# Kernel tuning notes

Measured on AMD Instinct MI355X. Metric: run time of the kernel, lower is better.

The kernel has to match this reference:

```python
import jax, jax.numpy as jnp
import numpy as np

B, N, L, D = 4096, 11, 12, 256
ZDIM = 32
LINE_DIM = 64
PAST_DIM = 6 * D - (2 * D + LINE_DIM)  # 960


def _pos_enc(length, d):
    # PositionalAgentEncoding.build_pos_enc
    pos = jnp.arange(length, dtype=jnp.float32)[:, None]
    div = jnp.exp(jnp.arange(0, d, 2, dtype=jnp.float32) * (-np.log(10000.0) / d))
    pe = jnp.zeros((length, d), dtype=jnp.float32)
    pe = pe.at[:, 0::2].set(jnp.sin(pos * div))
    pe = pe.at[:, 1::2].set(jnp.cos(pos * div))
    return pe


def setup_inputs() -> dict:
    key = jax.random.key(0)
    ks = jax.random.split(key, 16)
    s = 0.02
    return {
        "inputs": jax.random.normal(ks[0], (B * N, L, 4), jnp.float32),
        "past_feature": jax.random.normal(ks[1], (B * N, PAST_DIM), jnp.float32),
        "W_in": jax.random.normal(ks[2], (4, D), jnp.float32) * s,
        "b_in": jnp.zeros((D,), jnp.float32),
        "W_pos": jax.random.normal(ks[3], (2 * D, D), jnp.float32) * s,
        "b_pos": jnp.zeros((D,), jnp.float32),
        "W_fc2": jax.random.normal(ks[4], (L * D, D), jnp.float32) * s,
        "b_fc2": jnp.zeros((D,), jnp.float32),
        "W_fc3": jax.random.normal(ks[5], (D + N, D), jnp.float32) * s,
        "b_fc3": jnp.zeros((D,), jnp.float32),
        "W_msg": jax.random.normal(ks[6], (2 * D, D), jnp.float32) * s,
        "b_msg": jnp.zeros((D,), jnp.float32),
        "W_hyp": jax.random.normal(ks[7], (2 * D, D), jnp.float32) * s,
        "b_hyp": jnp.zeros((D,), jnp.float32),
        "W_line": jax.random.normal(ks[8], (D, LINE_DIM), jnp.float32) * s,
        "W_out": jax.random.normal(ks[9], (6 * D, 128), jnp.float32) * s,
        "b_out": jnp.zeros((128,), jnp.float32),
        "W_qz": jax.random.normal(ks[10], (128, 2 * ZDIM), jnp.float32) * s,
        "b_qz": jnp.zeros((2 * ZDIM,), jnp.float32),
        "batch_size": B,
        "agent_num": N,
    }


def reference(inputs, past_feature, W_in, b_in, W_pos, b_pos, W_fc2, b_fc2,
              W_fc3, b_fc3, W_msg, b_msg, W_hyp, b_hyp, W_line,
              W_out, b_out, W_qz, b_qz, batch_size, agent_num):
    BN, length, _ = inputs.shape
    d = W_in.shape[1]
    bsz, n = batch_size, agent_num
    # input_fc + positional encoding (concat=True, dropout=eval identity)
    tf = inputs @ W_in + b_in                                   # [BN, L, D]
    pe = jnp.broadcast_to(_pos_enc(length, d), (BN, length, d))
    tf = jnp.concatenate([tf, pe], axis=-1) @ W_pos + b_pos     # [BN, L, D]
    # input_fc2 over flattened time, then category concat + input_fc3
    ftraj = tf.reshape(bsz, n, length * d) @ W_fc2 + b_fc2      # [B, N, D]
    cat = jnp.broadcast_to(jnp.eye(n, dtype=ftraj.dtype), (bsz, n, n))
    ftraj = jnp.concatenate([ftraj, cat], axis=-1) @ W_fc3 + b_fc3
    # cosine correlation + per-scene adaptive threshold
    q = ftraj / jnp.linalg.norm(ftraj, axis=2, keepdims=True)
    corr = jnp.einsum('bnd,bmd->bnm', q, q)                     # [B, N, N]
    a = corr.min(axis=(1, 2))
    thr = jnp.where(a < 0.4, 0.4,
                    jnp.where((a > 0.4) & (a < 0.6), a + 0.1, a + 0.03))
    corr = jnp.where(corr < thr[:, None, None], 0.0, corr)
    # ordinary MS_HGNN surrogate: one dense message-passing round
    attn = jax.nn.softmax(jnp.einsum('bnd,bmd->bnm', ftraj, ftraj)
                          / jnp.sqrt(jnp.asarray(d, ftraj.dtype)), axis=-1)
    agg = jnp.einsum('bnm,bmd->bnd', attn, ftraj)
    ftraj_inter = jax.nn.relu(jnp.concatenate([ftraj, agg], -1) @ W_msg + b_msg)
    # hyper/clique surrogate: binarized thresholded corr as incidence, degree-normalized
    A = (corr > 0).astype(ftraj.dtype)
    A = A / jnp.maximum(A.sum(-1, keepdims=True), 1.0)
    hag = jnp.einsum('bnm,bmd->bnd', A, ftraj)
    hyp = jax.nn.relu(jnp.concatenate([ftraj, hag], -1) @ W_hyp + b_hyp)
    feat_bs = hyp @ W_line                                      # [B, N, 64]
    final = jnp.concatenate([ftraj, ftraj_inter, feat_bs], -1).reshape(bsz * n, -1)
    h = jnp.concatenate([past_feature, final], axis=-1)         # [BN, 6D]
    h = jax.nn.relu(h @ W_out + b_out)
    return h @ W_qz + b_qz                                      # [BN, 2*zdim]
```

## Files before the change

kernel.cpp:

```cpp
#include <hip/hip_runtime.h>
#include <hip/hip_bf16.h>

#define BB 4096
#define NNA 11
#define BN (BB*NNA)

#define OFF_WEFF   0
#define OFF_BIASL  1024
#define OFF_WBIG   4096
#define OFF_BIAS2  16384
#define OFF_WALL   16640
#define OFF_BIASN  28928
#define OFF_WG1F   31744
#define OFF_BIASG1 87040
#define OFF_WG2    99712
#define OFF_WQT    198656
#define OFF_P2T    202752
#define OFF_P3T    205824
#define OFF_MIX    296320
#define OFF_INTER  1287552

typedef short bh8 __attribute__((ext_vector_type(8)));
typedef float fx4 __attribute__((ext_vector_type(4)));

__device__ __forceinline__ float b2f(__hip_bfloat16 x) { return __bfloat162float(x); }
__device__ __forceinline__ short f2bs(float v) { __hip_bfloat16 h = __float2bfloat16(v); return *(short*)&h; }


__global__ __launch_bounds__(256) void k_p1(const float* W_in, const float* b_in,
                                            const float* W_pos, const float* b_pos,
                                            float* ws) {
  __shared__ float A[16*512];
  __shared__ float red[4*16*64];
  int t = threadIdx.x, cb = blockIdx.x;
  int ks = t >> 6, c = t & 63, col = cb*64 + c;
  float coef = -logf(10000.f) / 256.f;
  for (int i = t; i < 16*512; i += 256) {
    int row = i >> 9, kk = i & 511;
    float v;
    if (row < 4) v = (kk < 256) ? W_in[row*256 + kk] : 0.f;
    else if (kk < 256) v = b_in[kk];
    else {
      int ii = (kk - 256) >> 1;
      float dv = expf(coef * (float)(2*ii));
      float ang = (float)(row - 4) * dv;
      v = (kk & 1) ? cosf(ang) : sinf(ang);
    }
    A[i] = v;
  }
  __syncthreads();
  float acc[16];
  #pragma unroll
  for (int r = 0; r < 16; ++r) acc[r] = 0.f;
  #pragma unroll 4
  for (int j = 0; j < 128; ++j) {
    int jj = ks*128 + j;
    float b = W_pos[(size_t)jj*256 + col];
    #pragma unroll
    for (int r = 0; r < 16; ++r) acc[r] += A[r*512 + jj] * b;
  }
  #pragma unroll
  for (int r = 0; r < 16; ++r) red[(ks*16 + r)*64 + c] = acc[r];
  __syncthreads();
  for (int i = t; i < 16*64; i += 256) {
    int row = i >> 6, cc = i & 63;
    float s = red[row*64+cc] + red[(16+row)*64+cc] + red[(32+row)*64+cc] + red[(48+row)*64+cc];
    int gcol = cb*64 + cc;
    if (row < 4) ws[OFF_WEFF + row*256 + gcol] = s;
    else         ws[OFF_BIASL + (row-4)*256 + gcol] = s + b_pos[gcol];
  }
}

__global__ __launch_bounds__(256) void k_p2(const float* W_fc2, float* ws) {
  __shared__ float A[5*256];
  __shared__ float red[4*5*64];
  int t = threadIdx.x, cb = blockIdx.x, l = blockIdx.y;
  int ks = t >> 6, c = t & 63, col = cb*64 + c;
  for (int i = t; i < 5*256; i += 256) {
    int row = i >> 8, kk = i & 255;
    A[i] = (row < 4) ? ws[OFF_WEFF + row*256 + kk] : ws[OFF_BIASL + l*256 + kk];
  }
  __syncthreads();
  float acc[5] = {0.f, 0.f, 0.f, 0.f, 0.f};
  #pragma unroll 4
  for (int j = 0; j < 64; ++j) {
    int jj = ks*64 + j;
    float b = W_fc2[(size_t)(l*256 + jj)*256 + col];
    #pragma unroll
    for (int r = 0; r < 5; ++r) acc[r] += A[r*256 + jj] * b;
  }
  #pragma unroll
  for (int r = 0; r < 5; ++r) red[(ks*5 + r)*64 + c] = acc[r];
  __syncthreads();
  for (int i = t; i < 5*64; i += 256) {
    int row = i / 64, cc = i % 64;
    float s = red[row*64+cc] + red[(5+row)*64+cc] + red[(10+row)*64+cc] + red[(15+row)*64+cc];
    int gcol = cb*64 + cc;
    if (row < 4) ws[OFF_WBIG + (l*4 + row)*256 + gcol] = s;
    else         ws[OFF_P2T + l*256 + gcol] = s;
  }
}

__global__ __launch_bounds__(256) void k_p2b(const float* b_fc2, float* ws) {
  int d = threadIdx.x;
  float s = b_fc2[d];
  #pragma unroll
  for (int l = 0; l < 12; ++l) s += ws[OFF_P2T + l*256 + d];
  ws[OFF_BIAS2 + d] = s;
}

__global__ __launch_bounds__(256) void k_p3(const float* W_fc3, float* ws) {
  __shared__ float A[7*256];
  __shared__ float red[4*7*64];
  int t = threadIdx.x, cb = blockIdx.x, rg = blockIdx.y;
  int ks = t >> 6, c = t & 63, col = cb*64 + c;
  for (int i = t; i < 7*256; i += 256) {
    int row = i >> 8, kk = i & 255, gr = rg*7 + row;
    A[i] = (gr < 48) ? ws[OFF_WBIG + gr*256 + kk] : (gr == 48 ? ws[OFF_BIAS2 + kk] : 0.f);
  }
  __syncthreads();
  float acc[7] = {0.f,0.f,0.f,0.f,0.f,0.f,0.f};
  #pragma unroll 4
  for (int j = 0; j < 64; ++j) {
    int jj = ks*64 + j;
    float b = W_fc3[(size_t)jj*256 + col];
    #pragma unroll
    for (int r = 0; r < 7; ++r) acc[r] += A[r*256 + jj] * b;
  }
  #pragma unroll
  for (int r = 0; r < 7; ++r) red[(ks*7 + r)*64 + c] = acc[r];
  __syncthreads();
  for (int i = t; i < 7*64; i += 256) {
    int row = i / 64, cc = i % 64, gr = rg*7 + row;
    float s = red[row*64+cc] + red[(7+row)*64+cc] + red[(14+row)*64+cc] + red[(21+row)*64+cc];
    int gcol = cb*64 + cc;
    if (gr < 48)       ws[OFF_WALL + gr*256 + gcol] = s;
    else if (gr == 48) ws[OFF_P3T + gcol] = s;
  }
}

__global__ __launch_bounds__(256) void k_p3b(const float* W_fc3, const float* b_fc3, float* ws) {
  int d = threadIdx.x, n = blockIdx.x;
  ws[OFF_BIASN + n*256 + d] = ws[OFF_P3T + d] + b_fc3[d] + W_fc3[(size_t)(256+n)*256 + d];
}

__device__ __forceinline__ float wg1_elem(int j, int col, const float* W_msg,
                                          const float* W_hyp, const float* W_out) {
  if (col < 256)       return W_msg[j*256 + col];
  else if (col < 512)  return W_msg[(256+j)*256 + (col-256)];
  else if (col < 768)  return W_hyp[j*256 + (col-512)];
  else if (col < 1024) return W_hyp[(256+j)*256 + (col-768)];
  else                 return W_out[(960+j)*128 + (col-1024)];
}

__global__ __launch_bounds__(256) void k_p4(const float* W_msg, const float* b_msg,
                                            const float* W_hyp, const float* b_hyp,
                                            const float* W_out, float* ws) {
  __shared__ float A[8*256];
  __shared__ float red[4*8*64];
  int t = threadIdx.x, cb = blockIdx.x, rg = blockIdx.y;
  int ks = t >> 6, c = t & 63, col = cb*64 + c;
  for (int i = t; i < 8*256; i += 256) {
    int row = i >> 8, kk = i & 255, gr = rg*8 + row;
    A[i] = (gr < 48) ? ws[OFF_WALL + gr*256 + kk]
         : (gr < 59 ? ws[OFF_BIASN + (gr-48)*256 + kk] : 0.f);
  }
  __syncthreads();
  float acc[8];
  #pragma unroll
  for (int r = 0; r < 8; ++r) acc[r] = 0.f;
  #pragma unroll 4
  for (int j = 0; j < 64; ++j) {
    int jj = ks*64 + j;
    float b = wg1_elem(jj, col, W_msg, W_hyp, W_out);
    #pragma unroll
    for (int r = 0; r < 8; ++r) acc[r] += A[r*256 + jj] * b;
  }
  #pragma unroll
  for (int r = 0; r < 8; ++r) red[(ks*8 + r)*64 + c] = acc[r];
  __syncthreads();
  for (int i = t; i < 8*64; i += 256) {
    int row = i >> 6, cc = i & 63, gr = rg*8 + row;
    float s = red[row*64+cc] + red[(8+row)*64+cc] + red[(16+row)*64+cc] + red[(24+row)*64+cc];
    int gcol = cb*64 + cc;
    if (gr < 48) {
      ws[OFF_WG1F + gr*1152 + gcol] = s;
    } else if (gr < 59) {
      if (gcol < 256) s += b_msg[gcol];
      else if (gcol >= 512 && gcol < 768) s += b_hyp[gcol-512];
      ws[OFF_BIASG1 + (gr-48)*1152 + gcol] = s;
    }
  }
}

__global__ __launch_bounds__(128) void k_p5(const float* W_line, const float* W_out,
                                            float* ws) {
  int c = threadIdx.x, r = blockIdx.x;
  float v;
  if (r < 960)       v = W_out[r*128 + c];
  else if (r < 1216) v = W_out[(r+256)*128 + c];
  else if (r < 1472) {
    int dd = r - 1216;
    float s = 0.f;
    for (int j = 0; j < 64; ++j)
      s += W_line[dd*64 + j] * W_out[(1472+j)*128 + c];
    v = s;
  } else if (r < 1520) {
    v = ws[OFF_WG1F + (r-1472)*1152 + 1024 + c];
  } else v = 0.f;
  short* WTs = (short*)(ws + OFF_WG2);
  WTs[(size_t)c*1536 + r] = f2bs(v);
}

__global__ __launch_bounds__(256) void k_p6(const float* W_qz, float* ws) {
  int i = blockIdx.x*256 + threadIdx.x;
  int n = i >> 7, k = i & 127;
  short* WQs = (short*)(ws + OFF_WQT);
  WQs[n*128 + k] = f2bs(W_qz[k*64 + n]);
}

__global__ __launch_bounds__(256) void k_front(const float* inputs, float* ws) {
  __shared__ float XT[48*44];
  __shared__ float F[44*260];
  __shared__ float C[4*121];
  int t = threadIdx.x;
  int R0 = blockIdx.x * 44;
  for (int i = t; i < 44*48; i += 256) {
    int r = i / 48, k = i - r*48;
    XT[k*44 + r] = inputs[(size_t)(R0+r)*48 + k];
  }
  __syncthreads();
  {
    int d = t;
    float acc[44];
    #pragma unroll
    for (int r = 0; r < 44; ++r) acc[r] = ws[OFF_BIASN + (r % 11)*256 + d];
    for (int k = 0; k < 48; ++k) {
      float w = ws[OFF_WALL + k*256 + d];
      #pragma unroll
      for (int j = 0; j < 11; ++j) {
        float4 xv = *(const float4*)&XT[k*44 + 4*j];
        acc[4*j+0] += xv.x*w; acc[4*j+1] += xv.y*w;
        acc[4*j+2] += xv.z*w; acc[4*j+3] += xv.w*w;
      }
    }
    #pragma unroll
    for (int r = 0; r < 44; ++r) F[r*260 + d] = acc[r];
  }
  __syncthreads();
  int w = t >> 6, lane = t & 63;
  {
    const float4* F4 = (const float4*)F;
    for (int p = lane; p < 66; p += 64) {
      int n = 0, pp = p;
      while (pp >= 11 - n) { pp -= 11 - n; ++n; }
      int m = n + pp;
      int ra = (w*11 + n) * 65, rb2 = (w*11 + m) * 65;
      float s = 0.f;
      #pragma unroll 4
      for (int j = 0; j < 64; ++j) {
        float4 a = F4[ra + j], b = F4[rb2 + j];
        s += a.x*b.x + a.y*b.y + a.z*b.z + a.w*b.w;
      }
      C[w*121 + n*11 + m] = s;
      C[w*121 + m*11 + n] = s;
    }
  }
  __syncthreads();
  {
    float* Cw = C + w*121;
    float rn[11];
    #pragma unroll
    for (int n = 0; n < 11; ++n) rn[n] = 1.f / sqrtf(Cw[n*11+n]);
    float a = 1e30f;
    for (int n = 0; n < 11; ++n)
      for (int m = 0; m < 11; ++m)
        a = fminf(a, Cw[n*11+m] * rn[n] * rn[m]);
    float thr = (a < 0.4f) ? 0.4f : (((a > 0.4f) && (a < 0.6f)) ? a + 0.1f : a + 0.03f);
    int scene = blockIdx.x*4 + w;
    float* mixb = ws + OFF_MIX + (size_t)scene*242;
    if (lane < 11) {
      int n = lane;
      float mx = -1e30f;
      #pragma unroll
      for (int m = 0; m < 11; ++m) mx = fmaxf(mx, Cw[n*11+m]);
      mx *= (1.f/16.f);
      float e[11], ssum = 0.f;
      #pragma unroll
      for (int m = 0; m < 11; ++m) { e[m] = expf(Cw[n*11+m]*(1.f/16.f) - mx); ssum += e[m]; }
      float inv = 1.f / ssum;
      #pragma unroll
      for (int m = 0; m < 11; ++m) mixb[n*11+m] = e[m]*inv;
      float keep[11], cnt = 0.f;
      #pragma unroll
      for (int m = 0; m < 11; ++m) {
        float q = Cw[n*11+m] * rn[n] * rn[m];
        keep[m] = (q >= thr) ? 1.f : 0.f; cnt += keep[m];
      }
      float sc = 1.f / fmaxf(cnt, 1.f);
      #pragma unroll
      for (int m = 0; m < 11; ++m) mixb[121 + n*11 + m] = keep[m]*sc;
    }
  }
}

__global__ __launch_bounds__(256) void k_mix(const float* inputs, float* ws,
                                             __hip_bfloat16* outI, __hip_bfloat16* outH) {
  __shared__ float XT[48*24];
  __shared__ float MW[2*121];
  int t = threadIdx.x;
  int s0 = blockIdx.x * 2;
  int R0 = s0 * 11;
  int gy = blockIdx.y;
  __hip_bfloat16* dst = gy ? outH : outI;
  for (int i = t; i < 22*48; i += 256) {
    int r = i / 48, k = i - r*48;
    XT[k*24 + r] = inputs[(size_t)(R0+r)*48 + k];
  }
  for (int i = t; i < 96; i += 256) { int k = i >> 1, r = 22 + (i & 1); XT[k*24+r] = 0.f; }
  for (int i = t; i < 242; i += 256) {
    int s = i / 121, j = i - s*121;
    MW[i] = ws[OFF_MIX + (size_t)(s0+s)*242 + gy*121 + j];
  }
  __syncthreads();
  int gc = gy*512 + t;
  float accT[24], accB[24];
  #pragma unroll
  for (int r = 0; r < 24; ++r) {
    if (r < 22) {
      accT[r] = ws[OFF_BIASG1 + (r % 11)*1152 + gc];
      accB[r] = ws[OFF_BIASG1 + (r % 11)*1152 + gc + 256];
    } else { accT[r] = 0.f; accB[r] = 0.f; }
  }
  for (int k = 0; k < 48; ++k) {
    float wt = ws[OFF_WG1F + k*1152 + gc];
    float wb = ws[OFF_WG1F + k*1152 + gc + 256];
    #pragma unroll
    for (int j = 0; j < 6; ++j) {
      float4 xv = *(const float4*)&XT[k*24 + 4*j];
      accT[4*j+0] += xv.x*wt; accT[4*j+1] += xv.y*wt; accT[4*j+2] += xv.z*wt; accT[4*j+3] += xv.w*wt;
      accB[4*j+0] += xv.x*wb; accB[4*j+1] += xv.y*wb; accB[4*j+2] += xv.z*wb; accB[4*j+3] += xv.w*wb;
    }
  }
  #pragma unroll
  for (int s = 0; s < 2; ++s)
    #pragma unroll
    for (int n = 0; n < 11; ++n) {
      float v = accT[s*11+n];
      #pragma unroll
      for (int m = 0; m < 11; ++m)
        v += MW[s*121 + n*11 + m] * accB[s*11+m];
      v = fmaxf(v, 0.f);
      dst[(size_t)(R0 + s*11 + n)*256 + t] = __float2bfloat16(v);
    }
}

#define A_OFF 0
#define BT_OFF 4608
#define HS_OFF 0
#define WQ_OFF 8704
__global__ __launch_bounds__(256) void k_g2(const float* past, const float* inputs,
                                            const float* b_out, const float* b_qz,
                                            const __hip_bfloat16* interI, const __hip_bfloat16* hypI,
                                            float* ws, float* out) {
  __shared__ short LDS[18432];
  int t = threadIdx.x;
  int R0 = blockIdx.x * 64;
  int w = t >> 6, lane = t & 63, quad = lane >> 4, l16 = lane & 15;
  const short* WTs = (const short*)(ws + OFF_WG2);
  const short* WQs = (const short*)(ws + OFF_WQT);
  const short* intS = (const short*)interI;
  const short* hypS = (const short*)hypI;

  fx4 acc[4][2];
  #pragma unroll
  for (int mt = 0; mt < 4; ++mt)
    #pragma unroll
    for (int reg = 0; reg < 4; ++reg) {
      int nidx = (R0 + mt*16 + quad*4 + reg) % 11;
      #pragma unroll
      for (int nt = 0; nt < 2; ++nt) {
        int col = w*32 + nt*16 + l16;
        acc[mt][nt][reg] = b_out[col] + ws[OFF_BIASG1 + nidx*1152 + 1024 + col];
      }
    }

  int ar = t >> 2, akq = (t & 3) * 16;
  int bn = t >> 1, bkh = (t & 1) * 32;
  for (int ch = 0; ch < 24; ++ch) {
    __syncthreads();
    {
      short tmp[16];
      if (ch < 15) {
        const float4* sp = (const float4*)(past + (size_t)(R0+ar)*960 + ch*64 + akq);
        #pragma unroll
        for (int q = 0; q < 4; ++q) {
          float4 v = sp[q];
          tmp[4*q+0]=f2bs(v.x); tmp[4*q+1]=f2bs(v.y); tmp[4*q+2]=f2bs(v.z); tmp[4*q+3]=f2bs(v.w);
        }
        *(bh8*)&LDS[A_OFF + ar*72 + akq]     = *(bh8*)&tmp[0];
        *(bh8*)&LDS[A_OFF + ar*72 + akq + 8] = *(bh8*)&tmp[8];
      } else if (ch < 23) {
        const short* s = ((ch < 19) ? intS : hypS) + (size_t)(R0+ar)*256 + ((ch < 19) ? (ch-15) : (ch-19))*64 + akq;
        *(bh8*)&LDS[A_OFF + ar*72 + akq]     = *(const bh8*)&s[0];
        *(bh8*)&LDS[A_OFF + ar*72 + akq + 8] = *(const bh8*)&s[8];
      } else {
        if (akq < 48) {
          const float4* sp = (const float4*)(inputs + (size_t)(R0+ar)*48 + akq);
          #pragma unroll
          for (int q = 0; q < 4; ++q) {
            float4 v = sp[q];
            tmp[4*q+0]=f2bs(v.x); tmp[4*q+1]=f2bs(v.y); tmp[4*q+2]=f2bs(v.z); tmp[4*q+3]=f2bs(v.w);
          }
        } else {
          #pragma unroll
          for (int q = 0; q < 16; ++q) tmp[q] = 0;
        }
        *(bh8*)&LDS[A_OFF + ar*72 + akq]     = *(bh8*)&tmp[0];
        *(bh8*)&LDS[A_OFF + ar*72 + akq + 8] = *(bh8*)&tmp[8];
      }
    }
    {
      const short* s = WTs + (size_t)bn*1536 + ch*64 + bkh;
      #pragma unroll
      for (int q = 0; q < 4; ++q)
        *(bh8*)&LDS[BT_OFF + bn*72 + bkh + q*8] = *(const bh8*)&s[q*8];
    }
    __syncthreads();
    #pragma unroll
    for (int ks = 0; ks < 2; ++ks) {
      int kk = ks*32 + quad*8;
      bh8 a[4], b[2];
      #pragma unroll
      for (int mt = 0; mt < 4; ++mt) a[mt] = *(const bh8*)&LDS[A_OFF + (mt*16 + l16)*72 + kk];
      #pragma unroll
      for (int nt = 0; nt < 2; ++nt) b[nt] = *(const bh8*)&LDS[BT_OFF + (w*32 + nt*16 + l16)*72 + kk];
      #pragma unroll
      for (int mt = 0; mt < 4; ++mt)
        #pragma unroll
        for (int nt = 0; nt < 2; ++nt)
          acc[mt][nt] = __builtin_amdgcn_mfma_f32_16x16x32_bf16(a[mt], b[nt], acc[mt][nt], 0, 0, 0);
    }
  }
  __syncthreads();
  #pragma unroll
  for (int mt = 0; mt < 4; ++mt)
    #pragma unroll
    for (int nt = 0; nt < 2; ++nt)
      #pragma unroll
      for (int reg = 0; reg < 4; ++reg)
        LDS[HS_OFF + (mt*16 + quad*4 + reg)*136 + w*32 + nt*16 + l16] = f2bs(fmaxf(acc[mt][nt][reg], 0.f));
  {
    int n = t >> 2, kh = (t & 3) * 32;
    const short* s = WQs + n*128 + kh;
    #pragma unroll
    for (int q = 0; q < 4; ++q)
      *(bh8*)&LDS[WQ_OFF + n*136 + kh + q*8] = *(const bh8*)&s[q*8];
  }
  __syncthreads();
  fx4 acc2[4];
  {
    float bq = b_qz[w*16 + l16];
    #pragma unroll
    for (int mt = 0; mt < 4; ++mt) { acc2[mt][0]=bq; acc2[mt][1]=bq; acc2[mt][2]=bq; acc2[mt][3]=bq; }
  }
  #pragma unroll
  for (int ks = 0; ks < 4; ++ks) {
    int kk = ks*32 + quad*8;
    bh8 bb = *(const bh8*)&LDS[WQ_OFF + (w*16 + l16)*136 + kk];
    #pragma unroll
    for (int mt = 0; mt < 4; ++mt) {
      bh8 aa = *(const bh8*)&LDS[HS_OFF + (mt*16 + l16)*136 + kk];
      acc2[mt] = __builtin_amdgcn_mfma_f32_16x16x32_bf16(aa, bb, acc2[mt], 0, 0, 0);
    }
  }
  #pragma unroll
  for (int mt = 0; mt < 4; ++mt)
    #pragma unroll
    for (int reg = 0; reg < 4; ++reg)
      out[(size_t)(R0 + mt*16 + quad*4 + reg)*64 + w*16 + l16] = acc2[mt][reg];
}

extern "C" void kernel_launch(void* const* d_in, const int* in_sizes, int n_in,
                              void* d_out, int out_size, void* d_ws, size_t ws_size,
                              hipStream_t stream) {
  const float* inputs = (const float*)d_in[0];
  const float* past   = (const float*)d_in[1];
  const float* W_in   = (const float*)d_in[2];
  const float* b_in   = (const float*)d_in[3];
  const float* W_pos  = (const float*)d_in[4];
  const float* b_pos  = (const float*)d_in[5];
  const float* W_fc2  = (const float*)d_in[6];
  const float* b_fc2  = (const float*)d_in[7];
  const float* W_fc3  = (const float*)d_in[8];
  const float* b_fc3  = (const float*)d_in[9];
  const float* W_msg  = (const float*)d_in[10];
  const float* b_msg  = (const float*)d_in[11];
  const float* W_hyp  = (const float*)d_in[12];
  const float* b_hyp  = (const float*)d_in[13];
  const float* W_line = (const float*)d_in[14];
  const float* W_out  = (const float*)d_in[15];
  const float* b_out  = (const float*)d_in[16];
  const float* W_qz   = (const float*)d_in[17];
  const float* b_qz   = (const float*)d_in[18];
  float* ws = (float*)d_ws;
  __hip_bfloat16* interI = (__hip_bfloat16*)(ws + OFF_INTER);
  __hip_bfloat16* hypI   = interI + (size_t)BN*256;
  float* outp   = (float*)d_out;

  hipLaunchKernelGGL(k_p1,  dim3(4),      dim3(256), 0, stream, W_in, b_in, W_pos, b_pos, ws);
  hipLaunchKernelGGL(k_p2,  dim3(4, 12),  dim3(256), 0, stream, W_fc2, ws);
  hipLaunchKernelGGL(k_p2b, dim3(1),      dim3(256), 0, stream, b_fc2, ws);
  hipLaunchKernelGGL(k_p3,  dim3(4, 7),   dim3(256), 0, stream, W_fc3, ws);
  hipLaunchKernelGGL(k_p3b, dim3(11),     dim3(256), 0, stream, W_fc3, b_fc3, ws);
  hipLaunchKernelGGL(k_p4,  dim3(18, 8),  dim3(256), 0, stream, W_msg, b_msg, W_hyp, b_hyp, W_out, ws);
  hipLaunchKernelGGL(k_p5,  dim3(1536),   dim3(128), 0, stream, W_line, W_out, ws);
  hipLaunchKernelGGL(k_p6,  dim3(32),     dim3(256), 0, stream, W_qz, ws);
  hipLaunchKernelGGL(k_front, dim3(1024), dim3(256), 0, stream, inputs, ws);
  hipLaunchKernelGGL(k_mix, dim3(2048, 2), dim3(256), 0, stream, inputs, ws, interI, hypI);
  hipLaunchKernelGGL(k_g2,  dim3(704),    dim3(256), 0, stream, past, inputs, b_out, b_qz,
                     interI, hypI, ws, outp);
}
```

Baseline: 517.0 us.

## Double-buffer k_g2 GEMM with direct global-to-LDS loads and fold prep kernels

The main GEMM in k_g2 now double-buffers its A and B tiles in LDS. It uses XOR-swizzled layouts, stages the B operand with global_load_lds, and register-prefetches A two chunks ahead, so loads overlap the MFMA work and one barrier per chunk is removed. Separately, three small prep kernels (k_p2b, k_p3b, k_p6) are merged into their neighbours, which cuts kernel launches. The cost is more LDS per block, which may lower occupancy, and the bias sums are recomputed redundantly inside several kernels.

New measurement: 521.0 us. About the same (+0.8%).

```diff
diff --git a/kernel.cpp b/kernel.cpp
--- a/kernel.cpp
+++ b/kernel.cpp
@@ -23,8 +23,13 @@
 typedef short bh8 __attribute__((ext_vector_type(8)));
 typedef float fx4 __attribute__((ext_vector_type(4)));
 
-__device__ __forceinline__ float b2f(__hip_bfloat16 x) { return __bfloat162float(x); }
 __device__ __forceinline__ short f2bs(float v) { __hip_bfloat16 h = __float2bfloat16(v); return *(short*)&h; }
+
+typedef __attribute__((address_space(1))) const void __gptr_t;
+typedef __attribute__((address_space(3))) void __lptr_t;
+__device__ __forceinline__ void gload_lds16(const void* g, void* l) {
+  __builtin_amdgcn_global_load_lds((__gptr_t*)g, (__lptr_t*)l, 16, 0, 0);
+}
 
 
 __global__ __launch_bounds__(256) void k_p1(const float* W_in, const float* b_in,
@@ -101,22 +106,21 @@
   }
 }
 
-__global__ __launch_bounds__(256) void k_p2b(const float* b_fc2, float* ws) {
-  int d = threadIdx.x;
-  float s = b_fc2[d];
-  #pragma unroll
-  for (int l = 0; l < 12; ++l) s += ws[OFF_P2T + l*256 + d];
-  ws[OFF_BIAS2 + d] = s;
-}
-
-__global__ __launch_bounds__(256) void k_p3(const float* W_fc3, float* ws) {
+__global__ __launch_bounds__(256) void k_p3(const float* W_fc3, const float* b_fc2, float* ws) {
   __shared__ float A[7*256];
   __shared__ float red[4*7*64];
   int t = threadIdx.x, cb = blockIdx.x, rg = blockIdx.y;
   int ks = t >> 6, c = t & 63, col = cb*64 + c;
   for (int i = t; i < 7*256; i += 256) {
     int row = i >> 8, kk = i & 255, gr = rg*7 + row;
-    A[i] = (gr < 48) ? ws[OFF_WBIG + gr*256 + kk] : (gr == 48 ? ws[OFF_BIAS2 + kk] : 0.f);
+    float v;
+    if (gr < 48) v = ws[OFF_WBIG + gr*256 + kk];
+    else {
+      v = b_fc2[kk];
+      #pragma unroll
+      for (int l = 0; l < 12; ++l) v += ws[OFF_P2T + l*256 + kk];
+    }
+    A[i] = v;
   }
   __syncthreads();
   float acc[7] = {0.f,0.f,0.f,0.f,0.f,0.f,0.f};
@@ -137,11 +141,6 @@
     if (gr < 48)       ws[OFF_WALL + gr*256 + gcol] = s;
     else if (gr == 48) ws[OFF_P3T + gcol] = s;
   }
-}
-
-__global__ __launch_bounds__(256) void k_p3b(const float* W_fc3, const float* b_fc3, float* ws) {
-  int d = threadIdx.x, n = blockIdx.x;
-  ws[OFF_BIASN + n*256 + d] = ws[OFF_P3T + d] + b_fc3[d] + W_fc3[(size_t)(256+n)*256 + d];
 }
 
 __device__ __forceinline__ float wg1_elem(int j, int col, const float* W_msg,
@@ -155,15 +154,19 @@
 
 __global__ __launch_bounds__(256) void k_p4(const float* W_msg, const float* b_msg,
                                             const float* W_hyp, const float* b_hyp,
-                                            const float* W_out, float* ws) {
+                                            const float* W_out, const float* W_fc3,
+                                            const float* b_fc3, float* ws) {
   __shared__ float A[8*256];
   __shared__ float red[4*8*64];
   int t = threadIdx.x, cb = blockIdx.x, rg = blockIdx.y;
   int ks = t >> 6, c = t & 63, col = cb*64 + c;
   for (int i = t; i < 8*256; i += 256) {
     int row = i >> 8, kk = i & 255, gr = rg*8 + row;
-    A[i] = (gr < 48) ? ws[OFF_WALL + gr*256 + kk]
-         : (gr < 59 ? ws[OFF_BIASN + (gr-48)*256 + kk] : 0.f);
+    float v;
+    if (gr < 48)      v = ws[OFF_WALL + gr*256 + kk];
+    else if (gr < 59) v = ws[OFF_P3T + kk] + b_fc3[kk] + W_fc3[(size_t)(256 + gr - 48)*256 + kk];
+    else              v = 0.f;
+    A[i] = v;
   }
   __syncthreads();
   float acc[8];
@@ -194,8 +197,16 @@
 }
 
 __global__ __launch_bounds__(128) void k_p5(const float* W_line, const float* W_out,
-                                            float* ws) {
-  int c = threadIdx.x, r = blockIdx.x;
+                                            const float* W_qz, float* ws) {
+  int t = threadIdx.x;
+  if (blockIdx.x >= 1536) {
+    int i = (blockIdx.x - 1536)*128 + t;
+    int n = i >> 7, k = i & 127;
+    short* WQs = (short*)(ws + OFF_WQT);
+    WQs[n*128 + k] = f2bs(W_qz[k*64 + n]);
+    return;
+  }
+  int c = t, r = blockIdx.x;
   float v;
   if (r < 960)       v = W_out[r*128 + c];
   else if (r < 1216) v = W_out[(r+256)*128 + c];
@@ -212,14 +223,8 @@
   WTs[(size_t)c*1536 + r] = f2bs(v);
 }
 
-__global__ __launch_bounds__(256) void k_p6(const float* W_qz, float* ws) {
-  int i = blockIdx.x*256 + threadIdx.x;
-  int n = i >> 7, k = i & 127;
-  short* WQs = (short*)(ws + OFF_WQT);
-  WQs[n*128 + k] = f2bs(W_qz[k*64 + n]);
-}
-
-__global__ __launch_bounds__(256) void k_front(const float* inputs, float* ws) {
+__global__ __launch_bounds__(256) void k_front(const float* inputs, const float* W_fc3,
+                                               const float* b_fc3, float* ws) {
   __shared__ float XT[48*44];
   __shared__ float F[44*260];
   __shared__ float C[4*121];
@@ -233,8 +238,9 @@
   {
     int d = t;
     float acc[44];
-    #pragma unroll
-    for (int r = 0; r < 44; ++r) acc[r] = ws[OFF_BIASN + (r % 11)*256 + d];
+    float base = ws[OFF_P3T + d] + b_fc3[d];
+    #pragma unroll
+    for (int r = 0; r < 44; ++r) acc[r] = base + W_fc3[(size_t)(256 + (r % 11))*256 + d];
     for (int k = 0; k < 48; ++k) {
       float w = ws[OFF_WALL + k*256 + d];
       #pragma unroll
@@ -355,15 +361,18 @@
     }
 }
 
-#define A_OFF 0
-#define BT_OFF 4608
+#define A_BYTE(b) ((b)*8192)
+#define B_BYTE(b) (16384 + (b)*16384)
 #define HS_OFF 0
 #define WQ_OFF 8704
+__device__ __forceinline__ int swz(int row, int kshort) {
+  return row*128 + ((kshort*2) ^ ((row & 7) << 4));
+}
 __global__ __launch_bounds__(256) void k_g2(const float* past, const float* inputs,
                                             const float* b_out, const float* b_qz,
                                             const __hip_bfloat16* interI, const __hip_bfloat16* hypI,
                                             float* ws, float* out) {
-  __shared__ short LDS[18432];
+  __shared__ short LDS[24576];
   int t = threadIdx.x;
   int R0 = blockIdx.x * 64;
   int w = t >> 6, lane = t & 63, quad = lane >> 4, l16 = lane & 15;
@@ -371,6 +380,10 @@
   const short* WQs = (const short*)(ws + OFF_WQT);
   const short* intS = (const short*)interI;
   const short* hypS = (const short*)hypI;
+  char* LB = (char*)LDS;
+
+  int ar = t >> 2, akq = (t & 3) * 16;
+  int brr = lane >> 3, bb0 = (lane & 7) * 16;
 
   fx4 acc[4][2];
   #pragma unroll
@@ -385,62 +398,84 @@
       }
     }
 
-  int ar = t >> 2, akq = (t & 3) * 16;
-  int bn = t >> 1, bkh = (t & 1) * 32;
+  float4 pa[4];
+  bh8 pah[2];
+
+  auto prefA = [&](int cch) {
+    if (cch < 15) {
+      const float4* sp = (const float4*)(past + (size_t)(R0+ar)*960 + cch*64 + akq);
+      pa[0]=sp[0]; pa[1]=sp[1]; pa[2]=sp[2]; pa[3]=sp[3];
+    } else if (cch < 23) {
+      const short* s = ((cch < 19) ? intS : hypS) + (size_t)(R0+ar)*256 + ((cch < 19)?(cch-15):(cch-19))*64 + akq;
+      pah[0] = *(const bh8*)&s[0];
+      pah[1] = *(const bh8*)&s[8];
+    } else {
+      if (akq < 48) {
+        const float4* sp = (const float4*)(inputs + (size_t)(R0+ar)*48 + akq);
+        pa[0]=sp[0]; pa[1]=sp[1]; pa[2]=sp[2]; pa[3]=sp[3];
+      }
+    }
+  };
+  auto writeA = [&](int cch, int abuf) {
+    if (cch < 15 || cch == 23) {
+      short tmp[16];
+      if (cch == 23 && akq >= 48) {
+        #pragma unroll
+        for (int q = 0; q < 16; ++q) tmp[q] = 0;
+      } else {
+        #pragma unroll
+        for (int q = 0; q < 4; ++q) {
+          tmp[4*q+0]=f2bs(pa[q].x); tmp[4*q+1]=f2bs(pa[q].y);
+          tmp[4*q+2]=f2bs(pa[q].z); tmp[4*q+3]=f2bs(pa[q].w);
+        }
+      }
+      *(bh8*)(LB + A_BYTE(abuf) + swz(ar, akq))     = *(bh8*)&tmp[0];
+      *(bh8*)(LB + A_BYTE(abuf) + swz(ar, akq + 8)) = *(bh8*)&tmp[8];
+    } else {
+      *(bh8*)(LB + A_BYTE(abuf) + swz(ar, akq))     = pah[0];
+      *(bh8*)(LB + A_BYTE(abuf) + swz(ar, akq + 8)) = pah[1];
+    }
+  };
+  auto stageB = [&](int cch, int bbuf) {
+    #pragma unroll
+    for (int c = 0; c < 4; ++c) {
+      int r = (c*4 + w)*8 + brr;
+      const char* g = (const char*)(WTs + (size_t)r*1536 + cch*64) + (bb0 ^ ((r & 7) << 4));
+      gload_lds16(g, LB + B_BYTE(bbuf) + (c*4 + w)*1024);
+    }
+  };
+
+  prefA(0);
+  stageB(0, 0);
+  writeA(0, 0);
+  prefA(1);
+  int buf = 0;
   for (int ch = 0; ch < 24; ++ch) {
     __syncthreads();
-    {
-      short tmp[16];
-      if (ch < 15) {
-        const float4* sp = (const float4*)(past + (size_t)(R0+ar)*960 + ch*64 + akq);
-        #pragma unroll
-        for (int q = 0; q < 4; ++q) {
-          float4 v = sp[q];
-          tmp[4*q+0]=f2bs(v.x); tmp[4*q+1]=f2bs(v.y); tmp[4*q+2]=f2bs(v.z); tmp[4*q+3]=f2bs(v.w);
-        }
-        *(bh8*)&LDS[A_OFF + ar*72 + akq]     = *(bh8*)&tmp[0];
-        *(bh8*)&LDS[A_OFF + ar*72 + akq + 8] = *(bh8*)&tmp[8];
-      } else if (ch < 23) {
-        const short* s = ((ch < 19) ? intS : hypS) + (size_t)(R0+ar)*256 + ((ch < 19) ? (ch-15) : (ch-19))*64 + akq;
-        *(bh8*)&LDS[A_OFF + ar*72 + akq]     = *(const bh8*)&s[0];
-        *(bh8*)&LDS[A_OFF + ar*72 + akq + 8] = *(const bh8*)&s[8];
-      } else {
-        if (akq < 48) {
-          const float4* sp = (const float4*)(inputs + (size_t)(R0+ar)*48 + akq);
-          #pragma unroll
-          for (int q = 0; q < 4; ++q) {
-            float4 v = sp[q];
-            tmp[4*q+0]=f2bs(v.x); tmp[4*q+1]=f2bs(v.y); tmp[4*q+2]=f2bs(v.z); tmp[4*q+3]=f2bs(v.w);
-          }
-        } else {
-          #pragma unroll
-          for (int q = 0; q < 16; ++q) tmp[q] = 0;
-        }
-        *(bh8*)&LDS[A_OFF + ar*72 + akq]     = *(bh8*)&tmp[0];
-        *(bh8*)&LDS[A_OFF + ar*72 + akq + 8] = *(bh8*)&tmp[8];
-      }
-    }
-    {
-      const short* s = WTs + (size_t)bn*1536 + ch*64 + bkh;
-      #pragma unroll
-      for (int q = 0; q < 4; ++q)
-        *(bh8*)&LDS[BT_OFF + bn*72 + bkh + q*8] = *(const bh8*)&s[q*8];
-    }
-    __syncthreads();
+    if (ch + 1 < 24) {
+      stageB(ch + 1, buf ^ 1);
+      writeA(ch + 1, buf ^ 1);
+      if (ch + 2 < 24) prefA(ch + 2);
+    }
     #pragma unroll
     for (int ks = 0; ks < 2; ++ks) {
       int kk = ks*32 + quad*8;
       bh8 a[4], b[2];
       #pragma unroll
-      for (int mt = 0; mt < 4; ++mt) a[mt] = *(const bh8*)&LDS[A_OFF + (mt*16 + l16)*72 + kk];
-      #pragma unroll
-      for (int nt = 0; nt < 2; ++nt) b[nt] = *(const bh8*)&LDS[BT_OFF + (w*32 + nt*16 + l16)*72 + kk];
+      for (int mt = 0; mt < 4; ++mt)
+        a[mt] = *(const bh8*)(LB + A_BYTE(buf) + swz(mt*16 + l16, kk));
+      #pragma unroll
+      for (int nt = 0; nt < 2; ++nt) {
+        int r = w*32 + nt*16 + l16;
+        b[nt] = *(const bh8*)(LB + B_BYTE(buf) + swz(r, kk));
+      }
       #pragma unroll
       for (int mt = 0; mt < 4; ++mt)
         #pragma unroll
         for (int nt = 0; nt < 2; ++nt)
           acc[mt][nt] = __builtin_amdgcn_mfma_f32_16x16x32_bf16(a[mt], b[nt], acc[mt][nt], 0, 0, 0);
     }
+    buf ^= 1;
   }
   __syncthreads();
   #pragma unroll
@@ -510,13 +545,10 @@
 
   hipLaunchKernelGGL(k_p1,  dim3(4),      dim3(256), 0, stream, W_in, b_in, W_pos, b_pos, ws);
   hipLaunchKernelGGL(k_p2,  dim3(4, 12),  dim3(256), 0, stream, W_fc2, ws);
-  hipLaunchKernelGGL(k_p2b, dim3(1),      dim3(256), 0, stream, b_fc2, ws);
-  hipLaunchKernelGGL(k_p3,  dim3(4, 7),   dim3(256), 0, stream, W_fc3, ws);
-  hipLaunchKernelGGL(k_p3b, dim3(11),     dim3(256), 0, stream, W_fc3, b_fc3, ws);
-  hipLaunchKernelGGL(k_p4,  dim3(18, 8),  dim3(256), 0, stream, W_msg, b_msg, W_hyp, b_hyp, W_out, ws);
-  hipLaunchKernelGGL(k_p5,  dim3(1536),   dim3(128), 0, stream, W_line, W_out, ws);
-  hipLaunchKernelGGL(k_p6,  dim3(32),     dim3(256), 0, stream, W_qz, ws);
-  hipLaunchKernelGGL(k_front, dim3(1024), dim3(256), 0, stream, inputs, ws);
+  hipLaunchKernelGGL(k_p3,  dim3(4, 7),   dim3(256), 0, stream, W_fc3, b_fc2, ws);
+  hipLaunchKernelGGL(k_p4,  dim3(18, 8),  dim3(256), 0, stream, W_msg, b_msg, W_hyp, b_hyp, W_out, W_fc3, b_fc3, ws);
+  hipLaunchKernelGGL(k_p5,  dim3(1600),   dim3(128), 0, stream, W_line, W_out, W_qz, ws);
+  hipLaunchKernelGGL(k_front, dim3(1024), dim3(256), 0, stream, inputs, W_fc3, b_fc3, ws);
   hipLaunchKernelGGL(k_mix, dim3(2048, 2), dim3(256), 0, stream, inputs, ws, interI, hypI);
   hipLaunchKernelGGL(k_g2,  dim3(704),    dim3(256), 0, stream, past, inputs, b_out, b_qz,
                      interI, hypI, ws, outp);
```
